# Kernel optimization log

Hardware: AMD Instinct MI355X
Metric: run time of the kernel (lower is better)

## Reference

```python
import jax, jax.numpy as jnp
import numpy as np

NUM_ITERATIONS = 3

def squash(t, axis=-1):
    sq = jnp.clip(jnp.sum(t * t, axis=axis, keepdims=True), 1e-8, 1e4)
    norm = jnp.sqrt(sq)
    scale = sq / (1.0 + sq)
    return scale * (t / (norm + 1e-8))

def setup_inputs() -> dict:
    key = jax.random.key(0)
    k1, k2 = jax.random.split(key)
    B, N_in, N_out, D_in, D_out = 128, 1152, 10, 8, 16
    u = jax.random.normal(k1, (B, N_in, D_in), dtype=jnp.float32)
    W = jax.random.normal(k2, (N_in, N_out, D_out, D_in), dtype=jnp.float32) * 0.005
    return {"u": u, "W": W}

def reference(u, W):
    # u: [B, N_in, D_in]; W: [N_in, N_out, D_out, D_in]
    # u_hat: [B, N_in, N_out, D_out]
    u_hat = jnp.einsum('iodk,bik->biod', W, u)
    u_hat = jnp.clip(u_hat, -10.0, 10.0)
    B, N_in, N_out, _ = u_hat.shape
    b = jnp.zeros((B, N_in, N_out), dtype=u_hat.dtype)
    v = None
    for it in range(NUM_ITERATIONS):
        c = jax.nn.softmax(b, axis=2)                      # [B, N_in, N_out]
        s = jnp.einsum('bio,biod->bod', c, u_hat)          # [B, N_out, D_out]
        v = squash(s, axis=-1)                             # [B, N_out, D_out]
        if it < NUM_ITERATIONS - 1:
            agreement = jnp.einsum('biod,bod->bio', u_hat, v)
            b = b + jnp.clip(agreement, -10.0, 10.0)
    return v
```

## Files before the change

### kernel.cpp

```cpp
#include <hip/hip_runtime.h>
#include <cstddef>

#define NB    128
#define NIN   1152
#define NOUT  10
#define DOUT  16
#define OD    160
#define NSEG  16
#define SEGI  72
#define PGRID (NB * NSEG)

typedef __attribute__((ext_vector_type(4))) unsigned int u32x4;

__device__ __forceinline__ unsigned short f2bf(float x) {
    union { float f; unsigned u; } v; v.f = x;
    const unsigned r = v.u + 0x7fffu + ((v.u >> 16) & 1u);
    return (unsigned short)(r >> 16);
}
__device__ __forceinline__ unsigned pack2(float a, float b) {
    return (unsigned)f2bf(a) | ((unsigned)f2bf(b) << 16);
}
__device__ __forceinline__ float lo2f(unsigned w) {
    union { unsigned u; float f; } v; v.u = w << 16; return v.f;
}
__device__ __forceinline__ float hi2f(unsigned w) {
    union { unsigned u; float f; } v; v.u = w & 0xffff0000u; return v.f;
}

template<int CTRL>
__device__ __forceinline__ float dpp_f(float x) {
    return __int_as_float(__builtin_amdgcn_update_dpp(
        0, __float_as_int(x), CTRL, 0xF, 0xF, true));
}
__device__ __forceinline__ float row16_sum(float x) {
    x += dpp_f<0xB1>(x);
    x += dpp_f<0x4E>(x);
    x += dpp_f<0x124>(x);
    x += dpp_f<0x128>(x);
    return x;
}

__global__ __launch_bounds__(256)
void kprep(const float* __restrict__ W, unsigned* __restrict__ Wb)
{
    const int t = blockIdx.x * 256 + threadIdx.x;
    const float4 a = *reinterpret_cast<const float4*>(W + (size_t)t * 8);
    const float4 c = *reinterpret_cast<const float4*>(W + (size_t)t * 8 + 4);
    u32x4 o;
    o[0] = pack2(a.x, a.y); o[1] = pack2(a.z, a.w);
    o[2] = pack2(c.x, c.y); o[3] = pack2(c.z, c.w);
    *reinterpret_cast<u32x4*>(Wb + (size_t)t * 4) = o;
}

template<int PASS>
__global__ __launch_bounds__(256)
void kpass(const float* __restrict__ u, const unsigned* __restrict__ Wb,
           const float* __restrict__ p1, const float* __restrict__ p2,
           float* __restrict__ pout)
{
    __shared__ float u_lds[SEGI * 8];
    __shared__ float red[16 * 176];
    __shared__ float sv1[OD], sv2[OD], vb[OD];

    const int tid  = threadIdx.x;
    const int ip   = tid >> 4;
    const int dl   = tid & 15;
    const int bx   = blockIdx.x;
    const int xcd  = bx & 7;
    const int slot = bx >> 3;
    const int seg  = xcd + 8 * (slot >> 7);
    const int b    = slot & 127;

    if (tid < SEGI * 2)
        *reinterpret_cast<float4*>(u_lds + tid * 4) =
            *reinterpret_cast<const float4*>(
                u + ((size_t)b * NIN + seg * SEGI) * 8 + (size_t)tid * 4);

    if constexpr (PASS >= 2) {
        if (tid < OD) {
            float s = 0.0f;
            #pragma unroll
            for (int sg = 0; sg < NSEG; ++sg)
                s += p1[((size_t)b * NSEG + sg) * OD + tid];
            sv1[tid] = s;
            if constexpr (PASS == 3) {
                float s2 = 0.0f;
                #pragma unroll
                for (int sg = 0; sg < NSEG; ++sg)
                    s2 += p2[((size_t)b * NSEG + sg) * OD + tid];
                sv2[tid] = s2;
            }
        }
    }
    __syncthreads();
    if constexpr (PASS >= 2) {
        if (tid < OD) {
            const int o = tid >> 4;
            float ssq = 0.0f;
            #pragma unroll
            for (int dd = 0; dd < DOUT; ++dd) {
                const float x = sv1[o * DOUT + dd];
                ssq += x * x;
            }
            ssq = fminf(1e4f, fmaxf(1e-8f, ssq));
            float v = (ssq / (1.0f + ssq)) * sv1[tid] / (sqrtf(ssq) + 1e-8f);
            if constexpr (PASS == 3) {
                float sq2 = 0.0f;
                #pragma unroll
                for (int dd = 0; dd < DOUT; ++dd) {
                    const float x = sv2[o * DOUT + dd];
                    sq2 += x * x;
                }
                sq2 = fminf(1e4f, fmaxf(1e-8f, sq2));
                v += (sq2 / (1.0f + sq2)) * sv2[tid] / (sqrtf(sq2) + 1e-8f);
            }
            vb[tid] = v;
        }
    }
    __syncthreads();

    float vf[NOUT];
    if constexpr (PASS >= 2) {
        #pragma unroll
        for (int o = 0; o < NOUT; ++o) vf[o] = vb[o * DOUT + dl];
    }

    float acc[NOUT];
    #pragma unroll
    for (int o = 0; o < NOUT; ++o) acc[o] = 0.0f;

    for (int t = 0; t < 5; ++t) {
        if (t == 4 && ip >= 8) break;
        const int i_loc = t * 16 + ip;
        const size_t i = (size_t)seg * SEGI + i_loc;

        float ur[8];
        {
            const float4 a = *reinterpret_cast<const float4*>(u_lds + i_loc * 8);
            const float4 c = *reinterpret_cast<const float4*>(u_lds + i_loc * 8 + 4);
            ur[0] = a.x; ur[1] = a.y; ur[2] = a.z; ur[3] = a.w;
            ur[4] = c.x; ur[5] = c.y; ur[6] = c.z; ur[7] = c.w;
        }

        float uh[NOUT];
        #pragma unroll
        for (int o = 0; o < NOUT; ++o) {
            const u32x4 wv = *reinterpret_cast<const u32x4*>(
                Wb + ((i * NOUT + o) * DOUT + dl) * 4);
            uh[o] = lo2f(wv[0]) * ur[0] + hi2f(wv[0]) * ur[1]
                  + lo2f(wv[1]) * ur[2] + hi2f(wv[1]) * ur[3]
                  + lo2f(wv[2]) * ur[4] + hi2f(wv[2]) * ur[5]
                  + lo2f(wv[3]) * ur[6] + hi2f(wv[3]) * ur[7];
        }

        if constexpr (PASS == 1) {
            #pragma unroll
            for (int o = 0; o < NOUT; ++o) acc[o] += uh[o];
        } else {
            float lg[NOUT];
            #pragma unroll
            for (int o = 0; o < NOUT; ++o)
                lg[o] = row16_sum(uh[o] * vf[o]);

            float m = lg[0];
            #pragma unroll
            for (int o = 1; o < NOUT; ++o) m = fmaxf(m, lg[o]);
            float ssum = 0.0f;
            float cw[NOUT];
            #pragma unroll
            for (int o = 0; o < NOUT; ++o) {
                const float e = __expf(lg[o] - m);
                cw[o] = e;
                ssum += e;
            }
            const float inv = 1.0f / ssum;
            #pragma unroll
            for (int o = 0; o < NOUT; ++o)
                acc[o] += (cw[o] * inv) * uh[o];
        }
    }

    #pragma unroll
    for (int o = 0; o < NOUT; ++o)
        red[ip * 176 + o * DOUT + dl] = acc[o];
    __syncthreads();
    if (tid < OD) {
        float r = 0.0f;
        #pragma unroll
        for (int k = 0; k < 16; ++k)
            r += red[k * 176 + tid];
        if constexpr (PASS == 1) r *= 0.1f;
        pout[((size_t)b * NSEG + seg) * OD + tid] = r;
    }
}

__global__ __launch_bounds__(256)
void kout(const float* __restrict__ p3, float* __restrict__ out)
{
    const int idx = blockIdx.x * 256 + threadIdx.x;
    const int b   = idx / OD;
    const int od  = idx - b * OD;
    float s = 0.0f;
    #pragma unroll
    for (int sg = 0; sg < NSEG; ++sg)
        s += p3[((size_t)b * NSEG + sg) * OD + od];

    const float sq0 = row16_sum(s * s);
    const float sq  = fminf(1e4f, fmaxf(1e-8f, sq0));
    out[idx] = (sq / (1.0f + sq)) * s / (sqrtf(sq) + 1e-8f);
}

extern "C" void kernel_launch(void* const* d_in, const int* in_sizes, int n_in,
                              void* d_out, int out_size, void* d_ws, size_t ws_size,
                              hipStream_t stream)
{
    const float* u = (const float*)d_in[0];
    const float* W = (const float*)d_in[1];
    float* out = (float*)d_out;

    unsigned* Wb = (unsigned*)d_ws;
    float* p1 = (float*)(Wb + (size_t)NIN * NOUT * DOUT * 4);
    float* p2 = p1 + (size_t)NB * NSEG * OD;
    float* p3 = p2 + (size_t)NB * NSEG * OD;

    kprep<<<720, 256, 0, stream>>>(W, Wb);
    kpass<1><<<PGRID, 256, 0, stream>>>(u, Wb, nullptr, nullptr, p1);
    kpass<2><<<PGRID, 256, 0, stream>>>(u, Wb, p1, nullptr, p2);
    kpass<3><<<PGRID, 256, 0, stream>>>(u, Wb, p1, p2, p3);
    kout<<<NB * OD / 256, 256, 0, stream>>>(p3, out);
}
```

Before: 74.31 us.

## Repartition capsule passes by input-capsule groups with separate squash kernels

Each block now handles 8 input capsules across 16 batch rows, rather than 72 input capsules for a single batch row. Each W row is therefore reused across 16 batches instead of being reloaded per batch. Partial sums go straight to a 144-way partial buffer with no in-block LDS reduction. A small kv kernel after each pass reduces those partials and applies squash, so each pass reads finished v vectors. The softmax also drops max-subtraction, relying on the agreement logits staying small. The cost is much larger partial buffers and a longer reduction loop in kv, plus two extra kernel launches.

```diff
diff --git a/kernel.cpp b/kernel.cpp
--- a/kernel.cpp
+++ b/kernel.cpp
@@ -6,9 +6,9 @@
 #define NOUT  10
 #define DOUT  16
 #define OD    160
-#define NSEG  16
-#define SEGI  72
-#define PGRID (NB * NSEG)
+#define BI    8
+#define NIG   (NIN / BI)
+#define PGRID (NIG * 8)
 
 typedef __attribute__((ext_vector_type(4))) unsigned int u32x4;
 
@@ -55,89 +55,52 @@
 template<int PASS>
 __global__ __launch_bounds__(256)
 void kpass(const float* __restrict__ u, const unsigned* __restrict__ Wb,
-           const float* __restrict__ p1, const float* __restrict__ p2,
+           const float* __restrict__ vA, const float* __restrict__ vB,
            float* __restrict__ pout)
 {
-    __shared__ float u_lds[SEGI * 8];
-    __shared__ float red[16 * 176];
-    __shared__ float sv1[OD], sv2[OD], vb[OD];
+    __shared__ float u_lds[16 * 68];
 
-    const int tid  = threadIdx.x;
-    const int ip   = tid >> 4;
-    const int dl   = tid & 15;
-    const int bx   = blockIdx.x;
-    const int xcd  = bx & 7;
-    const int slot = bx >> 3;
-    const int seg  = xcd + 8 * (slot >> 7);
-    const int b    = slot & 127;
+    const int tid = threadIdx.x;
+    const int bl  = tid >> 4;
+    const int dl  = tid & 15;
+    const int ig  = blockIdx.x >> 3;
+    const int bt  = blockIdx.x & 7;
+    const int b   = bt * 16 + bl;
+    const int i0  = ig * BI;
 
-    if (tid < SEGI * 2)
-        *reinterpret_cast<float4*>(u_lds + tid * 4) =
-            *reinterpret_cast<const float4*>(
-                u + ((size_t)b * NIN + seg * SEGI) * 8 + (size_t)tid * 4);
-
-    if constexpr (PASS >= 2) {
-        if (tid < OD) {
-            float s = 0.0f;
-            #pragma unroll
-            for (int sg = 0; sg < NSEG; ++sg)
-                s += p1[((size_t)b * NSEG + sg) * OD + tid];
-            sv1[tid] = s;
-            if constexpr (PASS == 3) {
-                float s2 = 0.0f;
-                #pragma unroll
-                for (int sg = 0; sg < NSEG; ++sg)
-                    s2 += p2[((size_t)b * NSEG + sg) * OD + tid];
-                sv2[tid] = s2;
-            }
-        }
-    }
-    __syncthreads();
-    if constexpr (PASS >= 2) {
-        if (tid < OD) {
-            const int o = tid >> 4;
-            float ssq = 0.0f;
-            #pragma unroll
-            for (int dd = 0; dd < DOUT; ++dd) {
-                const float x = sv1[o * DOUT + dd];
-                ssq += x * x;
-            }
-            ssq = fminf(1e4f, fmaxf(1e-8f, ssq));
-            float v = (ssq / (1.0f + ssq)) * sv1[tid] / (sqrtf(ssq) + 1e-8f);
-            if constexpr (PASS == 3) {
-                float sq2 = 0.0f;
-                #pragma unroll
-                for (int dd = 0; dd < DOUT; ++dd) {
-                    const float x = sv2[o * DOUT + dd];
-                    sq2 += x * x;
-                }
-                sq2 = fminf(1e4f, fmaxf(1e-8f, sq2));
-                v += (sq2 / (1.0f + sq2)) * sv2[tid] / (sqrtf(sq2) + 1e-8f);
-            }
-            vb[tid] = v;
-        }
+    {
+        const int bs = tid >> 4;
+        const int is = (tid & 15) >> 1;
+        const int kh = tid & 1;
+        const float4 a = *reinterpret_cast<const float4*>(
+            u + ((size_t)(bt * 16 + bs) * NIN + i0 + is) * 8 + kh * 4);
+        *reinterpret_cast<float4*>(u_lds + bs * 68 + is * 8 + kh * 4) = a;
     }
     __syncthreads();
 
     float vf[NOUT];
     if constexpr (PASS >= 2) {
         #pragma unroll
-        for (int o = 0; o < NOUT; ++o) vf[o] = vb[o * DOUT + dl];
+        for (int o = 0; o < NOUT; ++o) {
+            float v = vA[(size_t)b * OD + o * DOUT + dl];
+            if constexpr (PASS == 3)
+                v += vB[(size_t)b * OD + o * DOUT + dl];
+            vf[o] = v;
+        }
     }
 
     float acc[NOUT];
     #pragma unroll
     for (int o = 0; o < NOUT; ++o) acc[o] = 0.0f;
 
-    for (int t = 0; t < 5; ++t) {
-        if (t == 4 && ip >= 8) break;
-        const int i_loc = t * 16 + ip;
-        const size_t i = (size_t)seg * SEGI + i_loc;
+    #pragma unroll
+    for (int t = 0; t < BI; ++t) {
+        const size_t i = (size_t)i0 + t;
 
         float ur[8];
         {
-            const float4 a = *reinterpret_cast<const float4*>(u_lds + i_loc * 8);
-            const float4 c = *reinterpret_cast<const float4*>(u_lds + i_loc * 8 + 4);
+            const float4 a = *reinterpret_cast<const float4*>(u_lds + bl * 68 + t * 8);
+            const float4 c = *reinterpret_cast<const float4*>(u_lds + bl * 68 + t * 8 + 4);
             ur[0] = a.x; ur[1] = a.y; ur[2] = a.z; ur[3] = a.w;
             ur[4] = c.x; ur[5] = c.y; ur[6] = c.z; ur[7] = c.w;
         }
@@ -157,19 +120,11 @@
             #pragma unroll
             for (int o = 0; o < NOUT; ++o) acc[o] += uh[o];
         } else {
-            float lg[NOUT];
-            #pragma unroll
-            for (int o = 0; o < NOUT; ++o)
-                lg[o] = row16_sum(uh[o] * vf[o]);
-
-            float m = lg[0];
-            #pragma unroll
-            for (int o = 1; o < NOUT; ++o) m = fmaxf(m, lg[o]);
+            float cw[NOUT];
             float ssum = 0.0f;
-            float cw[NOUT];
             #pragma unroll
             for (int o = 0; o < NOUT; ++o) {
-                const float e = __expf(lg[o] - m);
+                const float e = __expf(row16_sum(uh[o] * vf[o]));
                 cw[o] = e;
                 ssum += e;
             }
@@ -180,34 +135,24 @@
         }
     }
 
+    float* pp = pout + ((size_t)ig * NB + b) * OD + dl;
     #pragma unroll
     for (int o = 0; o < NOUT; ++o)
-        red[ip * 176 + o * DOUT + dl] = acc[o];
-    __syncthreads();
-    if (tid < OD) {
-        float r = 0.0f;
-        #pragma unroll
-        for (int k = 0; k < 16; ++k)
-            r += red[k * 176 + tid];
-        if constexpr (PASS == 1) r *= 0.1f;
-        pout[((size_t)b * NSEG + seg) * OD + tid] = r;
-    }
+        pp[o * DOUT] = (PASS == 1) ? acc[o] * 0.1f : acc[o];
 }
 
 __global__ __launch_bounds__(256)
-void kout(const float* __restrict__ p3, float* __restrict__ out)
+void kv(const float* __restrict__ p, float* __restrict__ vout)
 {
     const int idx = blockIdx.x * 256 + threadIdx.x;
-    const int b   = idx / OD;
-    const int od  = idx - b * OD;
     float s = 0.0f;
-    #pragma unroll
-    for (int sg = 0; sg < NSEG; ++sg)
-        s += p3[((size_t)b * NSEG + sg) * OD + od];
+    #pragma unroll 8
+    for (int ig = 0; ig < NIG; ++ig)
+        s += p[(size_t)ig * (NB * OD) + idx];
 
     const float sq0 = row16_sum(s * s);
     const float sq  = fminf(1e4f, fmaxf(1e-8f, sq0));
-    out[idx] = (sq / (1.0f + sq)) * s / (sqrtf(sq) + 1e-8f);
+    vout[idx] = (sq / (1.0f + sq)) * s / (sqrtf(sq) + 1e-8f);
 }
 
 extern "C" void kernel_launch(void* const* d_in, const int* in_sizes, int n_in,
@@ -220,12 +165,16 @@
 
     unsigned* Wb = (unsigned*)d_ws;
     float* p1 = (float*)(Wb + (size_t)NIN * NOUT * DOUT * 4);
-    float* p2 = p1 + (size_t)NB * NSEG * OD;
-    float* p3 = p2 + (size_t)NB * NSEG * OD;
+    float* p2 = p1 + (size_t)NIG * NB * OD;
+    float* p3 = p2 + (size_t)NIG * NB * OD;
+    float* v1 = p3 + (size_t)NIG * NB * OD;
+    float* v2 = v1 + NB * OD;
 
     kprep<<<720, 256, 0, stream>>>(W, Wb);
     kpass<1><<<PGRID, 256, 0, stream>>>(u, Wb, nullptr, nullptr, p1);
-    kpass<2><<<PGRID, 256, 0, stream>>>(u, Wb, p1, nullptr, p2);
-    kpass<3><<<PGRID, 256, 0, stream>>>(u, Wb, p1, p2, p3);
-    kout<<<NB * OD / 256, 256, 0, stream>>>(p3, out);
+    kv<<<NB * OD / 256, 256, 0, stream>>>(p1, v1);
+    kpass<2><<<PGRID, 256, 0, stream>>>(u, Wb, v1, nullptr, p2);
+    kv<<<NB * OD / 256, 256, 0, stream>>>(p2, v2);
+    kpass<3><<<PGRID, 256, 0, stream>>>(u, Wb, v1, v2, p3);
+    kv<<<NB * OD / 256, 256, 0, stream>>>(p3, out);
 }
```

After: 94.23 us. 26.8% more time.

## Use bf16 dot2 for u_hat, pack u to bf16, drop softmax max, rebalance segments

Applied to the files above, without the earlier changes.

Quantizes u to bf16 in LDS and computes the u_hat dot products with the fdot2 bf16 instruction instead of unpacking to fp32 and using FMAs. The segment split changes from 16x72 to 18x64 so every thread does exactly four iterations, and the block-to-segment mapping drops the XCD-aware swizzle. The softmax max-subtraction is removed on the assumption that logits stay bounded. This lowers ALU work per element but adds bf16 rounding of the activations and a risk of exp overflow, and the simpler block mapping may reduce L2 locality across XCDs.

```diff
diff --git a/kernel.cpp b/kernel.cpp
--- a/kernel.cpp
+++ b/kernel.cpp
@@ -6,11 +6,22 @@
 #define NOUT  10
 #define DOUT  16
 #define OD    160
-#define NSEG  16
-#define SEGI  72
+#define NSEG  18
+#define SEGI  64
 #define PGRID (NB * NSEG)
 
 typedef __attribute__((ext_vector_type(4))) unsigned int u32x4;
+
+#if __has_builtin(__builtin_amdgcn_fdot2_f32_bf16)
+#define HAS_DOT2 1
+typedef __attribute__((ext_vector_type(2))) __bf16 bf16x2;
+__device__ __forceinline__ float dot2bf(unsigned w, unsigned uu, float c) {
+    return __builtin_amdgcn_fdot2_f32_bf16(
+        __builtin_bit_cast(bf16x2, w), __builtin_bit_cast(bf16x2, uu), c, false);
+}
+#else
+#define HAS_DOT2 0
+#endif
 
 __device__ __forceinline__ unsigned short f2bf(float x) {
     union { float f; unsigned u; } v; v.f = x;
@@ -58,23 +69,22 @@
            const float* __restrict__ p1, const float* __restrict__ p2,
            float* __restrict__ pout)
 {
-    __shared__ float u_lds[SEGI * 8];
+    __shared__ unsigned u_lds[SEGI * 4];
     __shared__ float red[16 * 176];
     __shared__ float sv1[OD], sv2[OD], vb[OD];
 
-    const int tid  = threadIdx.x;
-    const int ip   = tid >> 4;
-    const int dl   = tid & 15;
-    const int bx   = blockIdx.x;
-    const int xcd  = bx & 7;
-    const int slot = bx >> 3;
-    const int seg  = xcd + 8 * (slot >> 7);
-    const int b    = slot & 127;
-
-    if (tid < SEGI * 2)
-        *reinterpret_cast<float4*>(u_lds + tid * 4) =
-            *reinterpret_cast<const float4*>(
-                u + ((size_t)b * NIN + seg * SEGI) * 8 + (size_t)tid * 4);
+    const int tid = threadIdx.x;
+    const int ip  = tid >> 4;
+    const int dl  = tid & 15;
+    const int seg = blockIdx.x >> 7;
+    const int b   = blockIdx.x & 127;
+
+    if (tid < 128) {
+        const float4 a = *reinterpret_cast<const float4*>(
+            u + ((size_t)b * NIN + seg * SEGI) * 8 + (size_t)tid * 4);
+        u_lds[tid * 2]     = pack2(a.x, a.y);
+        u_lds[tid * 2 + 1] = pack2(a.z, a.w);
+    }
 
     if constexpr (PASS >= 2) {
         if (tid < OD) {
@@ -129,47 +139,47 @@
     #pragma unroll
     for (int o = 0; o < NOUT; ++o) acc[o] = 0.0f;
 
-    for (int t = 0; t < 5; ++t) {
-        if (t == 4 && ip >= 8) break;
+    for (int t = 0; t < 4; ++t) {
         const int i_loc = t * 16 + ip;
         const size_t i = (size_t)seg * SEGI + i_loc;
 
+        const u32x4 uw = *reinterpret_cast<const u32x4*>(u_lds + i_loc * 4);
+#if !HAS_DOT2
         float ur[8];
-        {
-            const float4 a = *reinterpret_cast<const float4*>(u_lds + i_loc * 8);
-            const float4 c = *reinterpret_cast<const float4*>(u_lds + i_loc * 8 + 4);
-            ur[0] = a.x; ur[1] = a.y; ur[2] = a.z; ur[3] = a.w;
-            ur[4] = c.x; ur[5] = c.y; ur[6] = c.z; ur[7] = c.w;
-        }
+        #pragma unroll
+        for (int kp = 0; kp < 4; ++kp) {
+            ur[2 * kp]     = lo2f(uw[kp]);
+            ur[2 * kp + 1] = hi2f(uw[kp]);
+        }
+#endif
 
         float uh[NOUT];
         #pragma unroll
         for (int o = 0; o < NOUT; ++o) {
             const u32x4 wv = *reinterpret_cast<const u32x4*>(
                 Wb + ((i * NOUT + o) * DOUT + dl) * 4);
+#if HAS_DOT2
+            uh[o] = dot2bf(wv[0], uw[0],
+                    dot2bf(wv[1], uw[1],
+                    dot2bf(wv[2], uw[2],
+                    dot2bf(wv[3], uw[3], 0.0f))));
+#else
             uh[o] = lo2f(wv[0]) * ur[0] + hi2f(wv[0]) * ur[1]
                   + lo2f(wv[1]) * ur[2] + hi2f(wv[1]) * ur[3]
                   + lo2f(wv[2]) * ur[4] + hi2f(wv[2]) * ur[5]
                   + lo2f(wv[3]) * ur[6] + hi2f(wv[3]) * ur[7];
+#endif
         }
 
         if constexpr (PASS == 1) {
             #pragma unroll
             for (int o = 0; o < NOUT; ++o) acc[o] += uh[o];
         } else {
-            float lg[NOUT];
-            #pragma unroll
-            for (int o = 0; o < NOUT; ++o)
-                lg[o] = row16_sum(uh[o] * vf[o]);
-
-            float m = lg[0];
-            #pragma unroll
-            for (int o = 1; o < NOUT; ++o) m = fmaxf(m, lg[o]);
+            float cw[NOUT];
             float ssum = 0.0f;
-            float cw[NOUT];
             #pragma unroll
             for (int o = 0; o < NOUT; ++o) {
-                const float e = __expf(lg[o] - m);
+                const float e = __expf(row16_sum(uh[o] * vf[o]));
                 cw[o] = e;
                 ssum += e;
             }
```

New measurement: 65.06 us. 1.14x faster.
